# Kernel tuning notes

Hardware: AMD Instinct MI355X
Metric: run time of the kernel (lower is better)

## Reference

```python
import jax, jax.numpy as jnp
import numpy as np

FEAT_STRIDE = 16
NMS_THRESH = 0.7
PRE_NMS = 6000   # eval mode: n_test_pre_nms
POST_NMS = 300   # eval mode: n_test_post_nms
MIN_SIZE = 16
NEG = jnp.float32(-1e30)


def _base_anchors(base_size=16, ratios=(0.5, 1.0, 2.0), scales=(8, 16, 32)):
    ctr = (base_size - 1) / 2.0
    size = float(base_size * base_size)
    out = []
    for r in ratios:
        w = np.round(np.sqrt(size / r))
        h = np.round(w * r)
        for s in scales:
            ws, hs = w * s, h * s
            out.append([ctr - 0.5 * (ws - 1), ctr - 0.5 * (hs - 1),
                        ctr + 0.5 * (ws - 1), ctr + 0.5 * (hs - 1)])
    return np.asarray(out, dtype=np.float32)  # (9,4)


def _all_anchors(feat_h, feat_w):
    base = _base_anchors()
    sx = np.arange(feat_w, dtype=np.float32) * FEAT_STRIDE
    sy = np.arange(feat_h, dtype=np.float32) * FEAT_STRIDE
    gx, gy = np.meshgrid(sx, sy)                      # (H,W)
    shifts = np.stack([gx, gy, gx, gy], axis=-1).reshape(-1, 1, 4)
    anchors = (shifts + base[None, :, :]).reshape(-1, 4)  # (H*W*9,4), order (h,w,a)
    return jnp.asarray(anchors)


def _nms_keep(boxes):
    # boxes sorted by descending score; torchvision IoU convention (no +1)
    n = boxes.shape[0]
    area = (boxes[:, 2] - boxes[:, 0]) * (boxes[:, 3] - boxes[:, 1])
    lt = jnp.maximum(boxes[:, None, :2], boxes[None, :, :2])  # (N,N,2)
    rb = jnp.minimum(boxes[:, None, 2:], boxes[None, :, 2:])
    wh = jnp.clip(rb - lt, 0.0)
    inter = wh[..., 0] * wh[..., 1]
    iou = inter / (area[:, None] + area[None, :] - inter)
    over = iou > NMS_THRESH
    idx = jnp.arange(n)

    def body(i, supp):
        row = over[i] & (idx > i) & jnp.logical_not(supp[i])
        return supp | row

    supp = jax.lax.fori_loop(0, n, body, jnp.zeros((n,), bool))
    keep = jnp.nonzero(~supp, size=POST_NMS, fill_value=0)[0]
    return keep


def reference(rpn_cls_scores, rpn_bbox_preds, img_h, img_w):
    feat_h, feat_w = rpn_cls_scores.shape[2], rpn_cls_scores.shape[3]
    anchors = _all_anchors(feat_h, feat_w)                      # (K,4)
    scores = jax.nn.softmax(
        rpn_cls_scores.transpose(0, 2, 3, 1).reshape(-1, 2), axis=1)[:, 1]
    deltas = rpn_bbox_preds.transpose(0, 2, 3, 1).reshape(-1, 4)

    widths = anchors[:, 2] - anchors[:, 0] + 1.0
    heights = anchors[:, 3] - anchors[:, 1] + 1.0
    ctr_x = anchors[:, 0] + 0.5 * widths
    ctr_y = anchors[:, 1] + 0.5 * heights
    dx, dy, dw, dh = deltas[:, 0], deltas[:, 1], deltas[:, 2], deltas[:, 3]
    pcx = dx * widths + ctr_x
    pcy = dy * heights + ctr_y
    pw = jnp.exp(dw) * widths
    ph = jnp.exp(dh) * heights

    x1 = jnp.clip(pcx - 0.5 * pw, 0.0, img_w - 1)
    y1 = jnp.clip(pcy - 0.5 * ph, 0.0, img_h - 1)
    x2 = jnp.clip(pcx + 0.5 * pw, 0.0, img_w - 1)
    y2 = jnp.clip(pcy + 0.5 * ph, 0.0, img_h - 1)
    proposals = jnp.stack([x1, y1, x2, y2], axis=1)             # (K,4)

    valid = ((x2 - x1 + 1.0) >= MIN_SIZE) & ((y2 - y1 + 1.0) >= MIN_SIZE)
    masked = jnp.where(valid, scores, NEG)
    _, order = jax.lax.top_k(masked, PRE_NMS)                   # sort desc + pre-nms cut
    boxes = proposals[order]                                    # (PRE_NMS,4)

    keep = _nms_keep(boxes)
    kept = boxes[keep]                                          # (POST_NMS,4)
    batch_inds = jnp.zeros((POST_NMS, 1), dtype=kept.dtype)
    return jnp.concatenate([batch_inds, kept], axis=1)          # (POST_NMS,5)


def setup_inputs() -> dict:
    key = jax.random.key(0)
    k1, k2 = jax.random.split(key)
    rpn_cls_scores = jax.random.normal(k1, (1, 18, 64, 100), dtype=jnp.float32)
    rpn_bbox_preds = 0.2 * jax.random.normal(k2, (1, 36, 64, 100), dtype=jnp.float32)
    return {"rpn_cls_scores": rpn_cls_scores, "rpn_bbox_preds": rpn_bbox_preds,
            "img_h": 1024, "img_w": 1600}
```

## Files before the change

### kernel.cpp

```cpp
#include <hip/hip_runtime.h>

typedef unsigned long long u64;
typedef unsigned int u32;

#define FEAT_W 100
#define NANCH 9
#define NTOT 57600
#define NPAD 65536
#define PRE_NMS 6000
#define POST_NMS 300
#define NBLK 94
#define NCHUNK 24
#define CH_STRIDE 6400
#define CHUNK 1024
#define CAP 6144

__constant__ double c_base[9][4] = {
    {-84.0, -40.0, 99.0, 55.0},    {-176.0, -88.0, 191.0, 103.0},
    {-360.0, -184.0, 375.0, 199.0},{-56.0, -56.0, 71.0, 71.0},
    {-120.0, -120.0, 135.0, 135.0},{-248.0, -248.0, 263.0, 263.0},
    {-36.0, -80.0, 51.0, 95.0},    {-80.0, -168.0, 95.0, 183.0},
    {-168.0, -344.0, 183.0, 359.0}};

struct BoxD { double x1, y1, x2, y2; };

__device__ __forceinline__ int packed_off(int i) {
  int q = i >> 6, r = i & 63;
  return 94 * i - 32 * q * (q - 1) - r * q;
}

__device__ __forceinline__ BoxD decode_box(int i, const float* __restrict__ bbox,
                                           double imw1, double imh1) {
  int pos = i / NANCH;
  int a = i - pos * NANCH;
  int h = pos / FEAT_W;
  int w = pos - h * FEAT_W;
  double ax1 = c_base[a][0] + 16.0 * (double)w;
  double ay1 = c_base[a][1] + 16.0 * (double)h;
  double ax2 = c_base[a][2] + 16.0 * (double)w;
  double ay2 = c_base[a][3] + 16.0 * (double)h;
  double wd = ax2 - ax1 + 1.0;
  double hg = ay2 - ay1 + 1.0;
  double cx = ax1 + 0.5 * wd;
  double cy = ay1 + 0.5 * hg;
  const float* bp = bbox + (size_t)(4 * a) * CH_STRIDE + pos;
  double dx = (double)bp[0];
  double dy = (double)bp[CH_STRIDE];
  double dw = (double)bp[2 * CH_STRIDE];
  double dh = (double)bp[3 * CH_STRIDE];
  double pcx = dx * wd + cx;
  double pcy = dy * hg + cy;
  double pw = exp(dw) * wd;
  double ph = exp(dh) * hg;
  BoxD b;
  b.x1 = fmin(fmax(pcx - 0.5 * pw, 0.0), imw1);
  b.y1 = fmin(fmax(pcy - 0.5 * ph, 0.0), imh1);
  b.x2 = fmin(fmax(pcx + 0.5 * pw, 0.0), imw1);
  b.y2 = fmin(fmax(pcy + 0.5 * ph, 0.0), imh1);
  return b;
}

__device__ __forceinline__ u64 score_key(int i, const float* __restrict__ cls,
                                         const float* __restrict__ bbox,
                                         double imw1, double imh1) {
  BoxD b = decode_box(i, bbox, imw1, imh1);
  bool valid = (b.x2 - b.x1 + 1.0 >= 16.0) && (b.y2 - b.y1 + 1.0 >= 16.0);
  int pos = i / NANCH;
  int a = i - pos * NANCH;
  double c0 = (double)cls[(size_t)(2 * a) * CH_STRIDE + pos];
  double c1 = (double)cls[(size_t)(2 * a + 1) * CH_STRIDE + pos];
  double m = fmax(c0, c1);
  double e0 = exp(c0 - m), e1 = exp(c1 - m);
  double s = e1 / (e0 + e1);
  double masked = valid ? s : (double)(-1e30f);
  u64 u = (u64)__double_as_longlong(masked);
  return (u >> 63) ? ~u : (u | 0x8000000000000000ULL);
}

__device__ __forceinline__ bool before(u64 ka, u32 va, u64 kb, u32 vb) {
  return (ka > kb) || (ka == kb && va < vb);
}
__device__ __forceinline__ bool comes_after(u64 ka, u32 va, u64 kb, u32 vb) {
  return (ka < kb) || (ka == kb && va > vb);
}

__global__ __launch_bounds__(512) void k_score_sort(
    const float* __restrict__ cls, const float* __restrict__ bbox,
    const int* __restrict__ imh, const int* __restrict__ imw,
    u64* __restrict__ keys, u32* __restrict__ vals) {
  __shared__ u64 sk[CHUNK];
  __shared__ u32 sv[CHUNK];
  int base = blockIdx.x * CHUNK;
  double imh1 = (double)(imh[0] - 1);
  double imw1 = (double)(imw[0] - 1);
  for (int t = threadIdx.x; t < CHUNK; t += 512) {
    int i = base + t;
    if (i < NTOT) { sk[t] = score_key(i, cls, bbox, imw1, imh1); sv[t] = (u32)i; }
    else { sk[t] = 0ULL; sv[t] = (u32)i; }
  }
  __syncthreads();
  bool prev_cross = false;
  for (int k = 2; k <= CHUNK; k <<= 1) {
    for (int j = k >> 1; j > 0; j >>= 1) {
      bool cross = (j >= 128);
      if (cross || prev_cross) __syncthreads();
      int t = threadIdx.x;
      int i = ((t & ~(j - 1)) << 1) | (t & (j - 1));
      int l = i | j;
      bool up = ((i & k) == 0);
      u64 ka = sk[i], kb = sk[l];
      u32 va = sv[i], vb = sv[l];
      if (comes_after(ka, va, kb, vb) == up) { sk[i] = kb; sv[i] = vb; sk[l] = ka; sv[l] = va; }
      prev_cross = cross;
    }
  }
  __syncthreads();
  for (int t = threadIdx.x; t < CHUNK; t += 512) { keys[base + t] = sk[t]; vals[base + t] = sv[t]; }
}

__global__ void k_merge1(const u64* __restrict__ Ak, const u32* __restrict__ Av,
                         u64* __restrict__ Bk, u32* __restrict__ Bv) {
  int gtid = blockIdx.x * blockDim.x + threadIdx.x;
  if (gtid >= NPAD) return;
  int lst = gtid >> 10, pos = gtid & 1023, grp = lst >> 2;
  u64 k = Ak[gtid]; u32 v = Av[gtid];
  int b0 = grp << 2;
  int q = lst & 3;
  int i0 = 0 + (0 >= q), i1 = 1 + (1 >= q), i2 = 2 + (2 >= q);
  const u64* K0 = Ak + (size_t)(b0 + i0) * 1024;
  const u64* K1 = Ak + (size_t)(b0 + i1) * 1024;
  const u64* K2 = Ak + (size_t)(b0 + i2) * 1024;
  const u32* V0 = Av + (size_t)(b0 + i0) * 1024;
  const u32* V1 = Av + (size_t)(b0 + i1) * 1024;
  const u32* V2 = Av + (size_t)(b0 + i2) * 1024;
  int lo0 = 0, hi0 = 1024, lo1 = 0, hi1 = 1024, lo2 = 0, hi2 = 1024;
  #pragma unroll
  for (int st = 0; st < 11; ++st) {
    int m0 = (lo0 + hi0) >> 1, m1 = (lo1 + hi1) >> 1, m2 = (lo2 + hi2) >> 1;
    int c0 = min(m0, 1023), c1 = min(m1, 1023), c2 = min(m2, 1023);
    u64 k0 = K0[c0], k1 = K1[c1], k2 = K2[c2];
    u32 v0 = V0[c0], v1 = V1[c1], v2 = V2[c2];
    if (lo0 < hi0) { if (before(k0, v0, k, v)) lo0 = m0 + 1; else hi0 = m0; }
    if (lo1 < hi1) { if (before(k1, v1, k, v)) lo1 = m1 + 1; else hi1 = m1; }
    if (lo2 < hi2) { if (before(k2, v2, k, v)) lo2 = m2 + 1; else hi2 = m2; }
  }
  int rank = pos + lo0 + lo1 + lo2;
  Bk[(size_t)grp * 4096 + rank] = k;
  Bv[(size_t)grp * 4096 + rank] = v;
}

__global__ void k_merge2(const u64* __restrict__ Bk, const u32* __restrict__ Bv,
                         u64* __restrict__ Ak, u32* __restrict__ Av) {
  int gtid = blockIdx.x * blockDim.x + threadIdx.x;
  if (gtid >= NPAD) return;
  int lst = gtid >> 12, pos = gtid & 4095, grp = lst >> 2;
  u64 k = Bk[gtid]; u32 v = Bv[gtid];
  int b0 = grp << 2;
  int q = lst & 3;
  int i0 = 0 + (0 >= q), i1 = 1 + (1 >= q), i2 = 2 + (2 >= q);
  const u64* K0 = Bk + (size_t)(b0 + i0) * 4096;
  const u64* K1 = Bk + (size_t)(b0 + i1) * 4096;
  const u64* K2 = Bk + (size_t)(b0 + i2) * 4096;
  const u32* V0 = Bv + (size_t)(b0 + i0) * 4096;
  const u32* V1 = Bv + (size_t)(b0 + i1) * 4096;
  const u32* V2 = Bv + (size_t)(b0 + i2) * 4096;
  int lo0 = 0, hi0 = 4096, lo1 = 0, hi1 = 4096, lo2 = 0, hi2 = 4096;
  #pragma unroll
  for (int st = 0; st < 13; ++st) {
    int m0 = (lo0 + hi0) >> 1, m1 = (lo1 + hi1) >> 1, m2 = (lo2 + hi2) >> 1;
    int c0 = min(m0, 4095), c1 = min(m1, 4095), c2 = min(m2, 4095);
    u64 k0 = K0[c0], k1 = K1[c1], k2 = K2[c2];
    u32 v0 = V0[c0], v1 = V1[c1], v2 = V2[c2];
    if (lo0 < hi0) { if (before(k0, v0, k, v)) lo0 = m0 + 1; else hi0 = m0; }
    if (lo1 < hi1) { if (before(k1, v1, k, v)) lo1 = m1 + 1; else hi1 = m1; }
    if (lo2 < hi2) { if (before(k2, v2, k, v)) lo2 = m2 + 1; else hi2 = m2; }
  }
  int rank = pos + lo0 + lo1 + lo2;
  if (rank < CAP) { Ak[(size_t)grp * CAP + rank] = k; Av[(size_t)grp * CAP + rank] = v; }
}

__global__ void k_merge3(const u64* __restrict__ Ak, const u32* __restrict__ Av,
                         const float* __restrict__ bbox, const int* __restrict__ imh,
                         const int* __restrict__ imw, float4* __restrict__ fboxes) {
  int gtid = blockIdx.x * blockDim.x + threadIdx.x;
  if (gtid >= 4 * CAP) return;
  int lst = gtid / CAP, pos = gtid - lst * CAP;
  u64 k = Ak[gtid]; u32 v = Av[gtid];
  int i0 = 0 + (0 >= lst), i1 = 1 + (1 >= lst), i2 = 2 + (2 >= lst);
  const u64* K0 = Ak + (size_t)i0 * CAP;
  const u64* K1 = Ak + (size_t)i1 * CAP;
  const u64* K2 = Ak + (size_t)i2 * CAP;
  const u32* V0 = Av + (size_t)i0 * CAP;
  const u32* V1 = Av + (size_t)i1 * CAP;
  const u32* V2 = Av + (size_t)i2 * CAP;
  int lo0 = 0, hi0 = CAP, lo1 = 0, hi1 = CAP, lo2 = 0, hi2 = CAP;
  #pragma unroll
  for (int st = 0; st < 13; ++st) {
    int m0 = (lo0 + hi0) >> 1, m1 = (lo1 + hi1) >> 1, m2 = (lo2 + hi2) >> 1;
    int c0 = min(m0, CAP - 1), c1 = min(m1, CAP - 1), c2 = min(m2, CAP - 1);
    u64 k0 = K0[c0], k1 = K1[c1], k2 = K2[c2];
    u32 v0 = V0[c0], v1 = V1[c1], v2 = V2[c2];
    if (lo0 < hi0) { if (before(k0, v0, k, v)) lo0 = m0 + 1; else hi0 = m0; }
    if (lo1 < hi1) { if (before(k1, v1, k, v)) lo1 = m1 + 1; else hi1 = m1; }
    if (lo2 < hi2) { if (before(k2, v2, k, v)) lo2 = m2 + 1; else hi2 = m2; }
  }
  int rank = pos + lo0 + lo1 + lo2;
  if (rank < PRE_NMS) {
    double imh1 = (double)(imh[0] - 1);
    double imw1 = (double)(imw[0] - 1);
    BoxD b = decode_box((int)v, bbox, imw1, imh1);
    fboxes[rank] = make_float4((float)b.x1, (float)b.y1, (float)b.x2, (float)b.y2);
  }
}

__global__ void k_mask(const float4* __restrict__ fboxes, u64* __restrict__ mask,
                       u64* __restrict__ colC) {
  __shared__ float4 cb[64];
  int bc = blockIdx.x, br = blockIdx.y;
  int t = threadIdx.x;
  bool samechunk = (bc >> 2) == (br >> 2);
  if (bc < br) {
    if (samechunk) colC[(size_t)(((bc << 6) + t) * 4 + (br & 3))] = 0;
    return;
  }
  int j0 = bc * 64;
  int jt = j0 + t;
  cb[t] = (jt < PRE_NMS) ? fboxes[jt] : make_float4(0.f, 0.f, 0.f, 0.f);
  __syncthreads();
  int i = br * 64 + t;
  u64 bits = 0;
  if (i < PRE_NMS) {
    float4 rb = fboxes[i];
    float areai = (rb.z - rb.x) * (rb.w - rb.y);
    int cmax = min(64, PRE_NMS - j0);
    for (int c = 0; c < cmax; ++c) {
      int j = j0 + c;
      if (j <= i) continue;
      float4 cbx = cb[c];
      float xx1 = fmaxf(rb.x, cbx.x), yy1 = fmaxf(rb.y, cbx.y);
      float xx2 = fminf(rb.z, cbx.z), yy2 = fminf(rb.w, cbx.w);
      float w = fmaxf(xx2 - xx1, 0.0f), h = fmaxf(yy2 - yy1, 0.0f);
      float inter = w * h;
      float areaj = (cbx.z - cbx.x) * (cbx.w - cbx.y);
      float iou = inter / (areai + areaj - inter);
      if (iou > 0.7f) bits |= (1ULL << c);
    }
    mask[(size_t)(packed_off(i) + (bc - br))] = bits;
  }
  if (samechunk) {
    u64 colbits = 0;
    for (int j2 = 0; j2 < 64; ++j2) {
      u64 bl = __ballot(((bits >> j2) & 1ULL) != 0);
      if (t == j2) colbits = bl;
    }
    colC[(size_t)(((bc << 6) + t) * 4 + (br & 3))] = colbits;
  }
}

__device__ __forceinline__ u64 valid_word(int w) {
  int base = w << 6;
  if (base >= PRE_NMS) return 0ULL;
  if (base + 64 <= PRE_NMS) return ~0ULL;
  return (1ULL << (PRE_NMS - base)) - 1ULL;
}

__global__ __launch_bounds__(64) void k_scan(const u64* __restrict__ mask,
                                             const u64* __restrict__ colC,
                                             const float4* __restrict__ fboxes,
                                             float* __restrict__ out) {
  __shared__ int keepIdx[384];
  __shared__ int keepA[384];
  int lane = threadIdx.x;
  for (int r = lane; r < 384; r += 64) { keepIdx[r] = 0; keepA[r] = 0; }
  int nkeep = 0;
  bool done = false;
  int a0 = 0, a1 = 0, a2 = 0, a3 = 0, a4 = 0;
  u64 or0 = 0, or1 = 0, or2 = 0, or3 = 0;

  u64 ct00, ct01, ct02, ct03, ct10, ct11, ct12, ct13;
  u64 ct20, ct21, ct22, ct23, ct30, ct31, ct32, ct33;

#define COL_LOAD(cc, T, x0, x1, x2, x3)                                        \
  {                                                                            \
    int J_ = ((cc) << 8) + ((T) << 6) + lane;                                  \
    x0 = 0; x1 = 0; x2 = 0; x3 = 0;                                            \
    if (J_ < PRE_NMS) {                                                        \
      const ulonglong2* p_ = (const ulonglong2*)(colC + (size_t)J_ * 4);       \
      ulonglong2 u_ = p_[0], w_ = p_[1];                                       \
      x0 = u_.x; x1 = u_.y; x2 = w_.x; x3 = w_.y;                              \
    }                                                                          \
  }

  COL_LOAD(0, 0, ct00, ct01, ct02, ct03)
  COL_LOAD(0, 1, ct10, ct11, ct12, ct13)
  COL_LOAD(0, 2, ct20, ct21, ct22, ct23)
  COL_LOAD(0, 3, ct30, ct31, ct32, ct33)

  for (int c = 0; c < NCHUNK && !done; ++c) {
    int wbase = c << 2;
    int wnext = wbase + 4;
    bool gnext = (c + 1 < NCHUNK);
    bool tail_n = (wnext + 2) < NBLK;
    int oldn = nkeep;

    u64 n00 = 0, n01 = 0, n02 = 0, n03 = 0, n10 = 0, n11 = 0, n12 = 0, n13 = 0;
    u64 n20 = 0, n21 = 0, n22 = 0, n23 = 0, n30 = 0, n31 = 0, n32 = 0, n33 = 0;
    if (gnext) {
      COL_LOAD(c + 1, 0, n00, n01, n02, n03)
      COL_LOAD(c + 1, 1, n10, n11, n12, n13)
      COL_LOAD(c + 1, 2, n20, n21, n22, n23)
      COL_LOAD(c + 1, 3, n30, n31, n32, n33)
    }

    u64 e0 = 0, e1 = 0, e2 = 0, e3 = 0;
    if (gnext) {
#define EGATHER(AA, LIM)                                                       \
      if ((LIM) < oldn) {                                                      \
        const u64* p_ = mask + (size_t)(AA) + wnext;                           \
        e0 |= p_[0]; e1 |= p_[1];                                              \
        if (tail_n) { e2 |= p_[2]; e3 |= p_[3]; }                              \
      }
      EGATHER(a0, lane)
      EGATHER(a1, 64 + lane)
      EGATHER(a2, 128 + lane)
      EGATHER(a3, 192 + lane)
      EGATHER(a4, 256 + lane)
#undef EGATHER
    }

    u64 kf0 = 0, kf1 = 0, kf2 = 0, kf3 = 0;

#define RUN_WORD(OR_, TT, DIAGC, CROSS_EXPR, KFVAR)                            \
    if (!done) {                                                               \
      u64 alive = ~(OR_) & valid_word(wbase + (TT));                           \
      alive &= ~__ballot((CROSS_EXPR) != 0ULL);                                \
      u64 kfacc = 0;                                                           \
      while (alive) {                                                          \
        int b = __builtin_ctzll(alive);                                        \
        u64 bb = 1ULL << b;                                                    \
        kfacc |= bb;                                                           \
        u64 sup_ = __ballot((((DIAGC) >> b) & 1ULL) != 0ULL);                  \
        alive &= ~(sup_ | bb);                                                 \
      }                                                                        \
      KFVAR = kfacc;                                                           \
      if (kfacc) {                                                             \
        if ((kfacc >> lane) & 1ULL) {                                          \
          int idx = nkeep + __popcll(kfacc & ((1ULL << lane) - 1ULL));         \
          if (idx < 384) {                                                     \
            int K = (c << 8) + ((TT) << 6) + lane;                             \
            keepIdx[idx] = K;                                                  \
            keepA[idx] = packed_off(K) - (K >> 6);                             \
          }                                                                    \
        }                                                                      \
        nkeep += __popcll(kfacc);                                              \
        if (nkeep >= POST_NMS) done = true;                                    \
      }                                                                        \
    }

    RUN_WORD(or0, 0, ct00, 0ULL, kf0)
    RUN_WORD(or1, 1, ct11, (ct10 & kf0), kf1)
    RUN_WORD(or2, 2, ct22, (ct20 & kf0) | (ct21 & kf1), kf2)
    RUN_WORD(or3, 3, ct33, (ct30 & kf0) | (ct31 & kf1) | (ct32 & kf2), kf3)
#undef RUN_WORD
    (void)kf3;

    if (gnext && !done) {
      int nk = min(nkeep, 384);
#define LGATHER(AR, SLOT)                                                      \
      {                                                                        \
        int s_ = (SLOT);                                                       \
        if (s_ >= oldn && s_ < nk) {                                           \
          AR = keepA[s_];                                                      \
          const u64* p_ = mask + (size_t)AR + wnext;                           \
          e0 |= p_[0]; e1 |= p_[1];                                            \
          if (tail_n) { e2 |= p_[2]; e3 |= p_[3]; }                            \
        }                                                                      \
      }
      LGATHER(a0, lane)
      LGATHER(a1, 64 + lane)
      LGATHER(a2, 128 + lane)
      LGATHER(a3, 192 + lane)
      LGATHER(a4, 256 + lane)
#undef LGATHER
      #pragma unroll
      for (int m = 32; m; m >>= 1) {
        e0 |= __shfl_xor(e0, m);
        e1 |= __shfl_xor(e1, m);
        e2 |= __shfl_xor(e2, m);
        e3 |= __shfl_xor(e3, m);
      }
      or0 = e0; or1 = e1; or2 = e2; or3 = e3;
    }

    ct00 = n00; ct01 = n01; ct02 = n02; ct03 = n03;
    ct10 = n10; ct11 = n11; ct12 = n12; ct13 = n13;
    ct20 = n20; ct21 = n21; ct22 = n22; ct23 = n23;
    ct30 = n30; ct31 = n31; ct32 = n32; ct33 = n33;
  }
#undef COL_LOAD
  __syncthreads();

  for (int r = lane; r < POST_NMS; r += 64) {
    int kk = keepIdx[r];
    float4 b = fboxes[kk];
    float* o = out + r * 5;
    o[0] = 0.0f;
    o[1] = b.x;
    o[2] = b.y;
    o[3] = b.z;
    o[4] = b.w;
  }
}

extern "C" void kernel_launch(void* const* d_in, const int* in_sizes, int n_in,
                              void* d_out, int out_size, void* d_ws, size_t ws_size,
                              hipStream_t stream) {
  const float* cls = (const float*)d_in[0];
  const float* bbox = (const float*)d_in[1];
  const int* imh = (const int*)d_in[2];
  const int* imw = (const int*)d_in[3];
  float* out = (float*)d_out;

  char* p = (char*)d_ws;
  float4* fboxes = (float4*)p;
  u64* colC = (u64*)(p + 96256);
  char* mb = p + 385024;
  u64* maskbuf = (u64*)mb;
  u64* Ak = (u64*)mb;
  u32* Av = (u32*)(mb + 524288);
  u64* Bk = (u64*)(mb + 786432);
  u32* Bv = (u32*)(mb + 1310720);

  k_score_sort<<<64, 512, 0, stream>>>(cls, bbox, imh, imw, Ak, Av);
  k_merge1<<<NPAD / 256, 256, 0, stream>>>(Ak, Av, Bk, Bv);
  k_merge2<<<NPAD / 256, 256, 0, stream>>>(Bk, Bv, Ak, Av);
  k_merge3<<<(4 * CAP) / 256, 256, 0, stream>>>(Ak, Av, bbox, imh, imw, fboxes);
  k_mask<<<dim3(NBLK, NBLK), 64, 0, stream>>>(fboxes, maskbuf, colC);
  k_scan<<<1, 64, 0, stream>>>(maskbuf, colC, fboxes, out);
}
```

Measured before the change: 148.5 us.

## Fuse sort, merge, mask and scan stages into one cooperative kernel

Replaces the six separate launches (chunk sort, three merge passes, IoU mask, serial scan) with one cooperative kernel of 64 blocks × 512 threads, separating the stages with grid-wide syncs. The aim is to remove per-launch overhead and inter-kernel gaps. The mask stage now spreads its 94×94 tile jobs over 512 wavefronts in a loop instead of a large grid, which may cut its parallelism. Each grid.sync adds its own barrier cost.

```diff
diff --git a/kernel.cpp b/kernel.cpp
--- a/kernel.cpp
+++ b/kernel.cpp
@@ -1,4 +1,7 @@
 #include <hip/hip_runtime.h>
+#include <hip/hip_cooperative_groups.h>
+
+namespace cg = cooperative_groups;
 
 typedef unsigned long long u64;
 typedef unsigned int u32;
@@ -14,6 +17,8 @@
 #define CH_STRIDE 6400
 #define CHUNK 1024
 #define CAP 6144
+#define NBLOCKS 64
+#define NTHREADS 512
 
 __constant__ double c_base[9][4] = {
     {-84.0, -40.0, 99.0, 55.0},    {-176.0, -88.0, 191.0, 103.0},
@@ -84,177 +89,23 @@
   return (ka < kb) || (ka == kb && va > vb);
 }
 
-__global__ __launch_bounds__(512) void k_score_sort(
-    const float* __restrict__ cls, const float* __restrict__ bbox,
-    const int* __restrict__ imh, const int* __restrict__ imw,
-    u64* __restrict__ keys, u32* __restrict__ vals) {
-  __shared__ u64 sk[CHUNK];
-  __shared__ u32 sv[CHUNK];
-  int base = blockIdx.x * CHUNK;
-  double imh1 = (double)(imh[0] - 1);
-  double imw1 = (double)(imw[0] - 1);
-  for (int t = threadIdx.x; t < CHUNK; t += 512) {
-    int i = base + t;
-    if (i < NTOT) { sk[t] = score_key(i, cls, bbox, imw1, imh1); sv[t] = (u32)i; }
-    else { sk[t] = 0ULL; sv[t] = (u32)i; }
-  }
-  __syncthreads();
-  bool prev_cross = false;
-  for (int k = 2; k <= CHUNK; k <<= 1) {
-    for (int j = k >> 1; j > 0; j >>= 1) {
-      bool cross = (j >= 128);
-      if (cross || prev_cross) __syncthreads();
-      int t = threadIdx.x;
-      int i = ((t & ~(j - 1)) << 1) | (t & (j - 1));
-      int l = i | j;
-      bool up = ((i & k) == 0);
-      u64 ka = sk[i], kb = sk[l];
-      u32 va = sv[i], vb = sv[l];
-      if (comes_after(ka, va, kb, vb) == up) { sk[i] = kb; sv[i] = vb; sk[l] = ka; sv[l] = va; }
-      prev_cross = cross;
-    }
-  }
-  __syncthreads();
-  for (int t = threadIdx.x; t < CHUNK; t += 512) { keys[base + t] = sk[t]; vals[base + t] = sv[t]; }
-}
-
-__global__ void k_merge1(const u64* __restrict__ Ak, const u32* __restrict__ Av,
-                         u64* __restrict__ Bk, u32* __restrict__ Bv) {
-  int gtid = blockIdx.x * blockDim.x + threadIdx.x;
-  if (gtid >= NPAD) return;
-  int lst = gtid >> 10, pos = gtid & 1023, grp = lst >> 2;
-  u64 k = Ak[gtid]; u32 v = Av[gtid];
-  int b0 = grp << 2;
-  int q = lst & 3;
-  int i0 = 0 + (0 >= q), i1 = 1 + (1 >= q), i2 = 2 + (2 >= q);
-  const u64* K0 = Ak + (size_t)(b0 + i0) * 1024;
-  const u64* K1 = Ak + (size_t)(b0 + i1) * 1024;
-  const u64* K2 = Ak + (size_t)(b0 + i2) * 1024;
-  const u32* V0 = Av + (size_t)(b0 + i0) * 1024;
-  const u32* V1 = Av + (size_t)(b0 + i1) * 1024;
-  const u32* V2 = Av + (size_t)(b0 + i2) * 1024;
-  int lo0 = 0, hi0 = 1024, lo1 = 0, hi1 = 1024, lo2 = 0, hi2 = 1024;
+template <int N, int STEPS>
+__device__ __forceinline__ int rank3(const u64* __restrict__ K0, const u32* __restrict__ V0,
+                                     const u64* __restrict__ K1, const u32* __restrict__ V1,
+                                     const u64* __restrict__ K2, const u32* __restrict__ V2,
+                                     u64 k, u32 v) {
+  int lo0 = 0, hi0 = N, lo1 = 0, hi1 = N, lo2 = 0, hi2 = N;
   #pragma unroll
-  for (int st = 0; st < 11; ++st) {
+  for (int st = 0; st < STEPS; ++st) {
     int m0 = (lo0 + hi0) >> 1, m1 = (lo1 + hi1) >> 1, m2 = (lo2 + hi2) >> 1;
-    int c0 = min(m0, 1023), c1 = min(m1, 1023), c2 = min(m2, 1023);
+    int c0 = min(m0, N - 1), c1 = min(m1, N - 1), c2 = min(m2, N - 1);
     u64 k0 = K0[c0], k1 = K1[c1], k2 = K2[c2];
     u32 v0 = V0[c0], v1 = V1[c1], v2 = V2[c2];
     if (lo0 < hi0) { if (before(k0, v0, k, v)) lo0 = m0 + 1; else hi0 = m0; }
     if (lo1 < hi1) { if (before(k1, v1, k, v)) lo1 = m1 + 1; else hi1 = m1; }
     if (lo2 < hi2) { if (before(k2, v2, k, v)) lo2 = m2 + 1; else hi2 = m2; }
   }
-  int rank = pos + lo0 + lo1 + lo2;
-  Bk[(size_t)grp * 4096 + rank] = k;
-  Bv[(size_t)grp * 4096 + rank] = v;
-}
-
-__global__ void k_merge2(const u64* __restrict__ Bk, const u32* __restrict__ Bv,
-                         u64* __restrict__ Ak, u32* __restrict__ Av) {
-  int gtid = blockIdx.x * blockDim.x + threadIdx.x;
-  if (gtid >= NPAD) return;
-  int lst = gtid >> 12, pos = gtid & 4095, grp = lst >> 2;
-  u64 k = Bk[gtid]; u32 v = Bv[gtid];
-  int b0 = grp << 2;
-  int q = lst & 3;
-  int i0 = 0 + (0 >= q), i1 = 1 + (1 >= q), i2 = 2 + (2 >= q);
-  const u64* K0 = Bk + (size_t)(b0 + i0) * 4096;
-  const u64* K1 = Bk + (size_t)(b0 + i1) * 4096;
-  const u64* K2 = Bk + (size_t)(b0 + i2) * 4096;
-  const u32* V0 = Bv + (size_t)(b0 + i0) * 4096;
-  const u32* V1 = Bv + (size_t)(b0 + i1) * 4096;
-  const u32* V2 = Bv + (size_t)(b0 + i2) * 4096;
-  int lo0 = 0, hi0 = 4096, lo1 = 0, hi1 = 4096, lo2 = 0, hi2 = 4096;
-  #pragma unroll
-  for (int st = 0; st < 13; ++st) {
-    int m0 = (lo0 + hi0) >> 1, m1 = (lo1 + hi1) >> 1, m2 = (lo2 + hi2) >> 1;
-    int c0 = min(m0, 4095), c1 = min(m1, 4095), c2 = min(m2, 4095);
-    u64 k0 = K0[c0], k1 = K1[c1], k2 = K2[c2];
-    u32 v0 = V0[c0], v1 = V1[c1], v2 = V2[c2];
-    if (lo0 < hi0) { if (before(k0, v0, k, v)) lo0 = m0 + 1; else hi0 = m0; }
-    if (lo1 < hi1) { if (before(k1, v1, k, v)) lo1 = m1 + 1; else hi1 = m1; }
-    if (lo2 < hi2) { if (before(k2, v2, k, v)) lo2 = m2 + 1; else hi2 = m2; }
-  }
-  int rank = pos + lo0 + lo1 + lo2;
-  if (rank < CAP) { Ak[(size_t)grp * CAP + rank] = k; Av[(size_t)grp * CAP + rank] = v; }
-}
-
-__global__ void k_merge3(const u64* __restrict__ Ak, const u32* __restrict__ Av,
-                         const float* __restrict__ bbox, const int* __restrict__ imh,
-                         const int* __restrict__ imw, float4* __restrict__ fboxes) {
-  int gtid = blockIdx.x * blockDim.x + threadIdx.x;
-  if (gtid >= 4 * CAP) return;
-  int lst = gtid / CAP, pos = gtid - lst * CAP;
-  u64 k = Ak[gtid]; u32 v = Av[gtid];
-  int i0 = 0 + (0 >= lst), i1 = 1 + (1 >= lst), i2 = 2 + (2 >= lst);
-  const u64* K0 = Ak + (size_t)i0 * CAP;
-  const u64* K1 = Ak + (size_t)i1 * CAP;
-  const u64* K2 = Ak + (size_t)i2 * CAP;
-  const u32* V0 = Av + (size_t)i0 * CAP;
-  const u32* V1 = Av + (size_t)i1 * CAP;
-  const u32* V2 = Av + (size_t)i2 * CAP;
-  int lo0 = 0, hi0 = CAP, lo1 = 0, hi1 = CAP, lo2 = 0, hi2 = CAP;
-  #pragma unroll
-  for (int st = 0; st < 13; ++st) {
-    int m0 = (lo0 + hi0) >> 1, m1 = (lo1 + hi1) >> 1, m2 = (lo2 + hi2) >> 1;
-    int c0 = min(m0, CAP - 1), c1 = min(m1, CAP - 1), c2 = min(m2, CAP - 1);
-    u64 k0 = K0[c0], k1 = K1[c1], k2 = K2[c2];
-    u32 v0 = V0[c0], v1 = V1[c1], v2 = V2[c2];
-    if (lo0 < hi0) { if (before(k0, v0, k, v)) lo0 = m0 + 1; else hi0 = m0; }
-    if (lo1 < hi1) { if (before(k1, v1, k, v)) lo1 = m1 + 1; else hi1 = m1; }
-    if (lo2 < hi2) { if (before(k2, v2, k, v)) lo2 = m2 + 1; else hi2 = m2; }
-  }
-  int rank = pos + lo0 + lo1 + lo2;
-  if (rank < PRE_NMS) {
-    double imh1 = (double)(imh[0] - 1);
-    double imw1 = (double)(imw[0] - 1);
-    BoxD b = decode_box((int)v, bbox, imw1, imh1);
-    fboxes[rank] = make_float4((float)b.x1, (float)b.y1, (float)b.x2, (float)b.y2);
-  }
-}
-
-__global__ void k_mask(const float4* __restrict__ fboxes, u64* __restrict__ mask,
-                       u64* __restrict__ colC) {
-  __shared__ float4 cb[64];
-  int bc = blockIdx.x, br = blockIdx.y;
-  int t = threadIdx.x;
-  bool samechunk = (bc >> 2) == (br >> 2);
-  if (bc < br) {
-    if (samechunk) colC[(size_t)(((bc << 6) + t) * 4 + (br & 3))] = 0;
-    return;
-  }
-  int j0 = bc * 64;
-  int jt = j0 + t;
-  cb[t] = (jt < PRE_NMS) ? fboxes[jt] : make_float4(0.f, 0.f, 0.f, 0.f);
-  __syncthreads();
-  int i = br * 64 + t;
-  u64 bits = 0;
-  if (i < PRE_NMS) {
-    float4 rb = fboxes[i];
-    float areai = (rb.z - rb.x) * (rb.w - rb.y);
-    int cmax = min(64, PRE_NMS - j0);
-    for (int c = 0; c < cmax; ++c) {
-      int j = j0 + c;
-      if (j <= i) continue;
-      float4 cbx = cb[c];
-      float xx1 = fmaxf(rb.x, cbx.x), yy1 = fmaxf(rb.y, cbx.y);
-      float xx2 = fminf(rb.z, cbx.z), yy2 = fminf(rb.w, cbx.w);
-      float w = fmaxf(xx2 - xx1, 0.0f), h = fmaxf(yy2 - yy1, 0.0f);
-      float inter = w * h;
-      float areaj = (cbx.z - cbx.x) * (cbx.w - cbx.y);
-      float iou = inter / (areai + areaj - inter);
-      if (iou > 0.7f) bits |= (1ULL << c);
-    }
-    mask[(size_t)(packed_off(i) + (bc - br))] = bits;
-  }
-  if (samechunk) {
-    u64 colbits = 0;
-    for (int j2 = 0; j2 < 64; ++j2) {
-      u64 bl = __ballot(((bits >> j2) & 1ULL) != 0);
-      if (t == j2) colbits = bl;
-    }
-    colC[(size_t)(((bc << 6) + t) * 4 + (br & 3))] = colbits;
-  }
+  return lo0 + lo1 + lo2;
 }
 
 __device__ __forceinline__ u64 valid_word(int w) {
@@ -264,151 +115,297 @@
   return (1ULL << (PRE_NMS - base)) - 1ULL;
 }
 
-__global__ __launch_bounds__(64) void k_scan(const u64* __restrict__ mask,
-                                             const u64* __restrict__ colC,
-                                             const float4* __restrict__ fboxes,
-                                             float* __restrict__ out) {
+__global__ __launch_bounds__(NTHREADS) void k_all(
+    const float* __restrict__ cls, const float* __restrict__ bbox,
+    const int* __restrict__ imh, const int* __restrict__ imw,
+    float* __restrict__ out, float4* __restrict__ fboxes,
+    u64* __restrict__ colC, u64* __restrict__ mask,
+    u64* __restrict__ Ak, u32* __restrict__ Av,
+    u64* __restrict__ Bk, u32* __restrict__ Bv) {
+  cg::grid_group grid = cg::this_grid();
+  int bid = blockIdx.x;
+  int tid = threadIdx.x;
+
+  __shared__ u64 sk[CHUNK];
+  __shared__ u32 sv[CHUNK];
+  __shared__ float4 cbAll[8][64];
   __shared__ int keepIdx[384];
   __shared__ int keepA[384];
-  int lane = threadIdx.x;
-  for (int r = lane; r < 384; r += 64) { keepIdx[r] = 0; keepA[r] = 0; }
-  int nkeep = 0;
-  bool done = false;
-  int a0 = 0, a1 = 0, a2 = 0, a3 = 0, a4 = 0;
-  u64 or0 = 0, or1 = 0, or2 = 0, or3 = 0;
-
-  u64 ct00, ct01, ct02, ct03, ct10, ct11, ct12, ct13;
-  u64 ct20, ct21, ct22, ct23, ct30, ct31, ct32, ct33;
+
+  {
+    int base = bid * CHUNK;
+    double imh1 = (double)(imh[0] - 1);
+    double imw1 = (double)(imw[0] - 1);
+    for (int t = tid; t < CHUNK; t += NTHREADS) {
+      int i = base + t;
+      if (i < NTOT) { sk[t] = score_key(i, cls, bbox, imw1, imh1); sv[t] = (u32)i; }
+      else { sk[t] = 0ULL; sv[t] = (u32)i; }
+    }
+    __syncthreads();
+    bool prev_cross = false;
+    for (int k = 2; k <= CHUNK; k <<= 1) {
+      for (int j = k >> 1; j > 0; j >>= 1) {
+        bool cross = (j >= 128);
+        if (cross || prev_cross) __syncthreads();
+        int t = tid;
+        int i = ((t & ~(j - 1)) << 1) | (t & (j - 1));
+        int l = i | j;
+        bool up = ((i & k) == 0);
+        u64 ka = sk[i], kb = sk[l];
+        u32 va = sv[i], vb = sv[l];
+        if (comes_after(ka, va, kb, vb) == up) { sk[i] = kb; sv[i] = vb; sk[l] = ka; sv[l] = va; }
+        prev_cross = cross;
+      }
+    }
+    __syncthreads();
+    for (int t = tid; t < CHUNK; t += NTHREADS) { Ak[base + t] = sk[t]; Av[base + t] = sv[t]; }
+  }
+  grid.sync();
+
+  {
+    #pragma unroll
+    for (int half = 0; half < 2; ++half) {
+      int gtid = bid * NTHREADS + tid + half * (NBLOCKS * NTHREADS);
+      int lst = gtid >> 10, pos = gtid & 1023, grp = lst >> 2;
+      u64 k = Ak[gtid]; u32 v = Av[gtid];
+      int b0 = grp << 2, q = lst & 3;
+      int i0 = 0 + (0 >= q), i1 = 1 + (1 >= q), i2 = 2 + (2 >= q);
+      int rank = pos + rank3<1024, 11>(
+          Ak + (size_t)(b0 + i0) * 1024, Av + (size_t)(b0 + i0) * 1024,
+          Ak + (size_t)(b0 + i1) * 1024, Av + (size_t)(b0 + i1) * 1024,
+          Ak + (size_t)(b0 + i2) * 1024, Av + (size_t)(b0 + i2) * 1024, k, v);
+      Bk[(size_t)grp * 4096 + rank] = k;
+      Bv[(size_t)grp * 4096 + rank] = v;
+    }
+  }
+  grid.sync();
+
+  {
+    #pragma unroll
+    for (int half = 0; half < 2; ++half) {
+      int gtid = bid * NTHREADS + tid + half * (NBLOCKS * NTHREADS);
+      int lst = gtid >> 12, pos = gtid & 4095, grp = lst >> 2;
+      u64 k = Bk[gtid]; u32 v = Bv[gtid];
+      int b0 = grp << 2, q = lst & 3;
+      int i0 = 0 + (0 >= q), i1 = 1 + (1 >= q), i2 = 2 + (2 >= q);
+      int rank = pos + rank3<4096, 13>(
+          Bk + (size_t)(b0 + i0) * 4096, Bv + (size_t)(b0 + i0) * 4096,
+          Bk + (size_t)(b0 + i1) * 4096, Bv + (size_t)(b0 + i1) * 4096,
+          Bk + (size_t)(b0 + i2) * 4096, Bv + (size_t)(b0 + i2) * 4096, k, v);
+      if (rank < CAP) { Ak[(size_t)grp * CAP + rank] = k; Av[(size_t)grp * CAP + rank] = v; }
+    }
+  }
+  grid.sync();
+
+  {
+    int gtid = bid * NTHREADS + tid;
+    if (gtid < 4 * CAP) {
+      int lst = gtid / CAP, pos = gtid - lst * CAP;
+      u64 k = Ak[gtid]; u32 v = Av[gtid];
+      int i0 = 0 + (0 >= lst), i1 = 1 + (1 >= lst), i2 = 2 + (2 >= lst);
+      int rank = pos + rank3<CAP, 13>(
+          Ak + (size_t)i0 * CAP, Av + (size_t)i0 * CAP,
+          Ak + (size_t)i1 * CAP, Av + (size_t)i1 * CAP,
+          Ak + (size_t)i2 * CAP, Av + (size_t)i2 * CAP, k, v);
+      if (rank < PRE_NMS) {
+        double imh1 = (double)(imh[0] - 1);
+        double imw1 = (double)(imw[0] - 1);
+        BoxD b = decode_box((int)v, bbox, imw1, imh1);
+        fboxes[rank] = make_float4((float)b.x1, (float)b.y1, (float)b.x2, (float)b.y2);
+      }
+    }
+  }
+  grid.sync();
+
+  {
+    int w = tid >> 6, t = tid & 63;
+    float4* cbw = cbAll[w];
+    int gw = bid * 8 + w;
+    for (int job = gw; job < NBLK * NBLK; job += NBLOCKS * 8) {
+      int bc = job / NBLK, br = job - bc * NBLK;
+      bool samechunk = (bc >> 2) == (br >> 2);
+      if (bc < br) {
+        if (samechunk) colC[(size_t)(((bc << 6) + t) * 4 + (br & 3))] = 0;
+        continue;
+      }
+      int j0 = bc * 64;
+      int jt = j0 + t;
+      cbw[t] = (jt < PRE_NMS) ? fboxes[jt] : make_float4(0.f, 0.f, 0.f, 0.f);
+      int i = br * 64 + t;
+      u64 bits = 0;
+      if (i < PRE_NMS) {
+        float4 rb = fboxes[i];
+        float areai = (rb.z - rb.x) * (rb.w - rb.y);
+        int cmax = min(64, PRE_NMS - j0);
+        for (int c = 0; c < cmax; ++c) {
+          int j = j0 + c;
+          if (j <= i) continue;
+          float4 cbx = cbw[c];
+          float xx1 = fmaxf(rb.x, cbx.x), yy1 = fmaxf(rb.y, cbx.y);
+          float xx2 = fminf(rb.z, cbx.z), yy2 = fminf(rb.w, cbx.w);
+          float ww = fmaxf(xx2 - xx1, 0.0f), hh = fmaxf(yy2 - yy1, 0.0f);
+          float inter = ww * hh;
+          float areaj = (cbx.z - cbx.x) * (cbx.w - cbx.y);
+          float iou = inter / (areai + areaj - inter);
+          if (iou > 0.7f) bits |= (1ULL << c);
+        }
+        mask[(size_t)(packed_off(i) + (bc - br))] = bits;
+      }
+      if (samechunk) {
+        u64 colbits = 0;
+        for (int j2 = 0; j2 < 64; ++j2) {
+          u64 bl = __ballot(((bits >> j2) & 1ULL) != 0);
+          if (t == j2) colbits = bl;
+        }
+        colC[(size_t)(((bc << 6) + t) * 4 + (br & 3))] = colbits;
+      }
+    }
+  }
+  grid.sync();
+
+  if (bid == 0) {
+    for (int r = tid; r < 384; r += NTHREADS) { keepIdx[r] = 0; keepA[r] = 0; }
+    __syncthreads();
+    if (tid < 64) {
+      int lane = tid;
+      int nkeep = 0;
+      bool done = false;
+      int a0 = 0, a1 = 0, a2 = 0, a3 = 0, a4 = 0;
+      u64 or0 = 0, or1 = 0, or2 = 0, or3 = 0;
+
+      u64 ct00, ct01, ct02, ct03, ct10, ct11, ct12, ct13;
+      u64 ct20, ct21, ct22, ct23, ct30, ct31, ct32, ct33;
 
 #define COL_LOAD(cc, T, x0, x1, x2, x3)                                        \
-  {                                                                            \
-    int J_ = ((cc) << 8) + ((T) << 6) + lane;                                  \
-    x0 = 0; x1 = 0; x2 = 0; x3 = 0;                                            \
-    if (J_ < PRE_NMS) {                                                        \
-      const ulonglong2* p_ = (const ulonglong2*)(colC + (size_t)J_ * 4);       \
-      ulonglong2 u_ = p_[0], w_ = p_[1];                                       \
-      x0 = u_.x; x1 = u_.y; x2 = w_.x; x3 = w_.y;                              \
-    }                                                                          \
-  }
-
-  COL_LOAD(0, 0, ct00, ct01, ct02, ct03)
-  COL_LOAD(0, 1, ct10, ct11, ct12, ct13)
-  COL_LOAD(0, 2, ct20, ct21, ct22, ct23)
-  COL_LOAD(0, 3, ct30, ct31, ct32, ct33)
-
-  for (int c = 0; c < NCHUNK && !done; ++c) {
-    int wbase = c << 2;
-    int wnext = wbase + 4;
-    bool gnext = (c + 1 < NCHUNK);
-    bool tail_n = (wnext + 2) < NBLK;
-    int oldn = nkeep;
-
-    u64 n00 = 0, n01 = 0, n02 = 0, n03 = 0, n10 = 0, n11 = 0, n12 = 0, n13 = 0;
-    u64 n20 = 0, n21 = 0, n22 = 0, n23 = 0, n30 = 0, n31 = 0, n32 = 0, n33 = 0;
-    if (gnext) {
-      COL_LOAD(c + 1, 0, n00, n01, n02, n03)
-      COL_LOAD(c + 1, 1, n10, n11, n12, n13)
-      COL_LOAD(c + 1, 2, n20, n21, n22, n23)
-      COL_LOAD(c + 1, 3, n30, n31, n32, n33)
-    }
-
-    u64 e0 = 0, e1 = 0, e2 = 0, e3 = 0;
-    if (gnext) {
+      {                                                                        \
+        int J_ = ((cc) << 8) + ((T) << 6) + lane;                              \
+        x0 = 0; x1 = 0; x2 = 0; x3 = 0;                                        \
+        if (J_ < PRE_NMS) {                                                    \
+          const ulonglong2* p_ = (const ulonglong2*)(colC + (size_t)J_ * 4);   \
+          ulonglong2 u_ = p_[0], w_ = p_[1];                                   \
+          x0 = u_.x; x1 = u_.y; x2 = w_.x; x3 = w_.y;                          \
+        }                                                                      \
+      }
+
+      COL_LOAD(0, 0, ct00, ct01, ct02, ct03)
+      COL_LOAD(0, 1, ct10, ct11, ct12, ct13)
+      COL_LOAD(0, 2, ct20, ct21, ct22, ct23)
+      COL_LOAD(0, 3, ct30, ct31, ct32, ct33)
+
+      for (int c = 0; c < NCHUNK && !done; ++c) {
+        int wbase = c << 2;
+        int wnext = wbase + 4;
+        bool gnext = (c + 1 < NCHUNK);
+        bool tail_n = (wnext + 2) < NBLK;
+        int oldn = nkeep;
+
+        u64 n00 = 0, n01 = 0, n02 = 0, n03 = 0, n10 = 0, n11 = 0, n12 = 0, n13 = 0;
+        u64 n20 = 0, n21 = 0, n22 = 0, n23 = 0, n30 = 0, n31 = 0, n32 = 0, n33 = 0;
+        if (gnext) {
+          COL_LOAD(c + 1, 0, n00, n01, n02, n03)
+          COL_LOAD(c + 1, 1, n10, n11, n12, n13)
+          COL_LOAD(c + 1, 2, n20, n21, n22, n23)
+          COL_LOAD(c + 1, 3, n30, n31, n32, n33)
+        }
+
+        u64 e0 = 0, e1 = 0, e2 = 0, e3 = 0;
+        if (gnext) {
 #define EGATHER(AA, LIM)                                                       \
-      if ((LIM) < oldn) {                                                      \
-        const u64* p_ = mask + (size_t)(AA) + wnext;                           \
-        e0 |= p_[0]; e1 |= p_[1];                                              \
-        if (tail_n) { e2 |= p_[2]; e3 |= p_[3]; }                              \
-      }
-      EGATHER(a0, lane)
-      EGATHER(a1, 64 + lane)
-      EGATHER(a2, 128 + lane)
-      EGATHER(a3, 192 + lane)
-      EGATHER(a4, 256 + lane)
+          if ((LIM) < oldn) {                                                  \
+            const u64* p_ = mask + (size_t)(AA) + wnext;                       \
+            e0 |= p_[0]; e1 |= p_[1];                                          \
+            if (tail_n) { e2 |= p_[2]; e3 |= p_[3]; }                          \
+          }
+          EGATHER(a0, lane)
+          EGATHER(a1, 64 + lane)
+          EGATHER(a2, 128 + lane)
+          EGATHER(a3, 192 + lane)
+          EGATHER(a4, 256 + lane)
 #undef EGATHER
-    }
-
-    u64 kf0 = 0, kf1 = 0, kf2 = 0, kf3 = 0;
+        }
+
+        u64 kf0 = 0, kf1 = 0, kf2 = 0, kf3 = 0;
 
 #define RUN_WORD(OR_, TT, DIAGC, CROSS_EXPR, KFVAR)                            \
-    if (!done) {                                                               \
-      u64 alive = ~(OR_) & valid_word(wbase + (TT));                           \
-      alive &= ~__ballot((CROSS_EXPR) != 0ULL);                                \
-      u64 kfacc = 0;                                                           \
-      while (alive) {                                                          \
-        int b = __builtin_ctzll(alive);                                        \
-        u64 bb = 1ULL << b;                                                    \
-        kfacc |= bb;                                                           \
-        u64 sup_ = __ballot((((DIAGC) >> b) & 1ULL) != 0ULL);                  \
-        alive &= ~(sup_ | bb);                                                 \
-      }                                                                        \
-      KFVAR = kfacc;                                                           \
-      if (kfacc) {                                                             \
-        if ((kfacc >> lane) & 1ULL) {                                          \
-          int idx = nkeep + __popcll(kfacc & ((1ULL << lane) - 1ULL));         \
-          if (idx < 384) {                                                     \
-            int K = (c << 8) + ((TT) << 6) + lane;                             \
-            keepIdx[idx] = K;                                                  \
-            keepA[idx] = packed_off(K) - (K >> 6);                             \
+        if (!done) {                                                           \
+          u64 alive = ~(OR_) & valid_word(wbase + (TT));                       \
+          alive &= ~__ballot((CROSS_EXPR) != 0ULL);                            \
+          u64 kfacc = 0;                                                       \
+          while (alive) {                                                      \
+            int b = __builtin_ctzll(alive);                                    \
+            u64 bb = 1ULL << b;                                                \
+            kfacc |= bb;                                                       \
+            u64 sup_ = __ballot((((DIAGC) >> b) & 1ULL) != 0ULL);              \
+            alive &= ~(sup_ | bb);                                             \
           }                                                                    \
-        }                                                                      \
-        nkeep += __popcll(kfacc);                                              \
-        if (nkeep >= POST_NMS) done = true;                                    \
-      }                                                                        \
-    }
-
-    RUN_WORD(or0, 0, ct00, 0ULL, kf0)
-    RUN_WORD(or1, 1, ct11, (ct10 & kf0), kf1)
-    RUN_WORD(or2, 2, ct22, (ct20 & kf0) | (ct21 & kf1), kf2)
-    RUN_WORD(or3, 3, ct33, (ct30 & kf0) | (ct31 & kf1) | (ct32 & kf2), kf3)
+          KFVAR = kfacc;                                                       \
+          if (kfacc) {                                                         \
+            if ((kfacc >> lane) & 1ULL) {                                      \
+              int idx = nkeep + __popcll(kfacc & ((1ULL << lane) - 1ULL));     \
+              if (idx < 384) {                                                 \
+                int K = (c << 8) + ((TT) << 6) + lane;                         \
+                keepIdx[idx] = K;                                              \
+                keepA[idx] = packed_off(K) - (K >> 6);                         \
+              }                                                                \
+            }                                                                  \
+            nkeep += __popcll(kfacc);                                          \
+            if (nkeep >= POST_NMS) done = true;                                \
+          }                                                                    \
+        }
+
+        RUN_WORD(or0, 0, ct00, 0ULL, kf0)
+        RUN_WORD(or1, 1, ct11, (ct10 & kf0), kf1)
+        RUN_WORD(or2, 2, ct22, (ct20 & kf0) | (ct21 & kf1), kf2)
+        RUN_WORD(or3, 3, ct33, (ct30 & kf0) | (ct31 & kf1) | (ct32 & kf2), kf3)
 #undef RUN_WORD
-    (void)kf3;
-
-    if (gnext && !done) {
-      int nk = min(nkeep, 384);
+        (void)kf3;
+
+        if (gnext && !done) {
+          int nk = min(nkeep, 384);
 #define LGATHER(AR, SLOT)                                                      \
-      {                                                                        \
-        int s_ = (SLOT);                                                       \
-        if (s_ >= oldn && s_ < nk) {                                           \
-          AR = keepA[s_];                                                      \
-          const u64* p_ = mask + (size_t)AR + wnext;                           \
-          e0 |= p_[0]; e1 |= p_[1];                                            \
-          if (tail_n) { e2 |= p_[2]; e3 |= p_[3]; }                            \
-        }                                                                      \
-      }
-      LGATHER(a0, lane)
-      LGATHER(a1, 64 + lane)
-      LGATHER(a2, 128 + lane)
-      LGATHER(a3, 192 + lane)
-      LGATHER(a4, 256 + lane)
+          {                                                                    \
+            int s_ = (SLOT);                                                   \
+            if (s_ >= oldn && s_ < nk) {                                       \
+              AR = keepA[s_];                                                  \
+              const u64* p_ = mask + (size_t)AR + wnext;                       \
+              e0 |= p_[0]; e1 |= p_[1];                                        \
+              if (tail_n) { e2 |= p_[2]; e3 |= p_[3]; }                        \
+            }                                                                  \
+          }
+          LGATHER(a0, lane)
+          LGATHER(a1, 64 + lane)
+          LGATHER(a2, 128 + lane)
+          LGATHER(a3, 192 + lane)
+          LGATHER(a4, 256 + lane)
 #undef LGATHER
-      #pragma unroll
-      for (int m = 32; m; m >>= 1) {
-        e0 |= __shfl_xor(e0, m);
-        e1 |= __shfl_xor(e1, m);
-        e2 |= __shfl_xor(e2, m);
-        e3 |= __shfl_xor(e3, m);
-      }
-      or0 = e0; or1 = e1; or2 = e2; or3 = e3;
-    }
-
-    ct00 = n00; ct01 = n01; ct02 = n02; ct03 = n03;
-    ct10 = n10; ct11 = n11; ct12 = n12; ct13 = n13;
-    ct20 = n20; ct21 = n21; ct22 = n22; ct23 = n23;
-    ct30 = n30; ct31 = n31; ct32 = n32; ct33 = n33;
-  }
+          #pragma unroll
+          for (int m = 32; m; m >>= 1) {
+            e0 |= __shfl_xor(e0, m);
+            e1 |= __shfl_xor(e1, m);
+            e2 |= __shfl_xor(e2, m);
+            e3 |= __shfl_xor(e3, m);
+          }
+          or0 = e0; or1 = e1; or2 = e2; or3 = e3;
+        }
+
+        ct00 = n00; ct01 = n01; ct02 = n02; ct03 = n03;
+        ct10 = n10; ct11 = n11; ct12 = n12; ct13 = n13;
+        ct20 = n20; ct21 = n21; ct22 = n22; ct23 = n23;
+        ct30 = n30; ct31 = n31; ct32 = n32; ct33 = n33;
+      }
 #undef COL_LOAD
-  __syncthreads();
-
-  for (int r = lane; r < POST_NMS; r += 64) {
-    int kk = keepIdx[r];
-    float4 b = fboxes[kk];
-    float* o = out + r * 5;
-    o[0] = 0.0f;
-    o[1] = b.x;
-    o[2] = b.y;
-    o[3] = b.z;
-    o[4] = b.w;
+    }
+    __syncthreads();
+    for (int r = tid; r < POST_NMS; r += NTHREADS) {
+      int kk = keepIdx[r];
+      float4 b = fboxes[kk];
+      float* o = out + r * 5;
+      o[0] = 0.0f;
+      o[1] = b.x;
+      o[2] = b.y;
+      o[3] = b.z;
+      o[4] = b.w;
+    }
   }
 }
 
@@ -431,10 +428,9 @@
   u64* Bk = (u64*)(mb + 786432);
   u32* Bv = (u32*)(mb + 1310720);
 
-  k_score_sort<<<64, 512, 0, stream>>>(cls, bbox, imh, imw, Ak, Av);
-  k_merge1<<<NPAD / 256, 256, 0, stream>>>(Ak, Av, Bk, Bv);
-  k_merge2<<<NPAD / 256, 256, 0, stream>>>(Bk, Bv, Ak, Av);
-  k_merge3<<<(4 * CAP) / 256, 256, 0, stream>>>(Ak, Av, bbox, imh, imw, fboxes);
-  k_mask<<<dim3(NBLK, NBLK), 64, 0, stream>>>(fboxes, maskbuf, colC);
-  k_scan<<<1, 64, 0, stream>>>(maskbuf, colC, fboxes, out);
-}
+  void* args[] = {(void*)&cls, (void*)&bbox, (void*)&imh, (void*)&imw,
+                  (void*)&out, (void*)&fboxes, (void*)&colC, (void*)&maskbuf,
+                  (void*)&Ak, (void*)&Av, (void*)&Bk, (void*)&Bv};
+  hipLaunchCooperativeKernel((const void*)k_all, dim3(NBLOCKS), dim3(NTHREADS),
+                             args, 0, stream);
+}
```

New measurement: 291.5 us. 96.3% more time.
